# Kernel optimization log

Measured on AMD Instinct MI355X. Metric: run time of the kernel, lower is better.

Reference implementation:

```python
import jax, jax.numpy as jnp
import numpy as np

B, C, CI, H, W = 4, 256, 128, 64, 64  # batch, in_channels, inter_channels, spatial


def conv1x1(x, w, b):
    # x: [B,C,H,W], w: [O,C], b: [O] -> [B,O,H,W]
    return jnp.einsum('bchw,oc->bohw', x, w) + b[None, :, None, None]


def setup_inputs() -> dict:
    key = jax.random.key(0)
    ks = jax.random.split(key, 9)
    s = 0.02
    return {
        'x':  jax.random.normal(ks[0], (B, C, H, W), dtype=jnp.float32),
        'Wg': jax.random.normal(ks[1], (CI, C), dtype=jnp.float32) * s,
        'bg': jnp.zeros((CI,), dtype=jnp.float32),
        'Wt': jax.random.normal(ks[2], (CI, C), dtype=jnp.float32) * s,
        'bt': jnp.zeros((CI,), dtype=jnp.float32),
        'Wp': jax.random.normal(ks[3], (CI, C), dtype=jnp.float32) * s,
        'bp': jnp.zeros((CI,), dtype=jnp.float32),
        'Wo': jax.random.normal(ks[4], (C, CI), dtype=jnp.float32) * s,
        'bo': jnp.zeros((C,), dtype=jnp.float32),
    }


def reference(x, Wg, bg, Wt, bt, Wp, bp, Wo, bo):
    b, c, h, w = x.shape
    n = h * w
    g  = conv1x1(x, Wg, bg).reshape(b, -1, n)   # [B,CI,N]
    th = conv1x1(x, Wt, bt).reshape(b, -1, n)   # [B,CI,N]
    ph = conv1x1(x, Wp, bp).reshape(b, -1, n)   # [B,CI,N]
    f = jnp.einsum('bci,bcj->bij', th, ph)      # [B,N,N] unscaled scores
    a = jax.nn.softmax(f, axis=-1)
    y = jnp.einsum('bij,bcj->bci', a, g)        # [B,CI,N]
    y = y.reshape(b, -1, h, w)
    return conv1x1(y, Wo, bo) + x
```

## Files before the change

kernel.cpp:

```cpp
#include <hip/hip_runtime.h>
#include <math.h>

#define B_  4
#define C_  256
#define CI_ 128
#define N_  4096

typedef short s16x8  __attribute__((ext_vector_type(8)));
typedef float f32x4  __attribute__((ext_vector_type(4)));
typedef float f32x16 __attribute__((ext_vector_type(16)));

__device__ inline ushort f2bf(float f) {
    unsigned int u = __float_as_uint(f);
    u += 0x7FFF + ((u >> 16) & 1);
    return (ushort)(u >> 16);
}
__device__ inline float bf2f(ushort u) {
    return __uint_as_float(((unsigned int)u) << 16);
}

__device__ inline unsigned pkbf(float a, float b) {
    unsigned r;
    asm("v_cvt_pk_bf16_f32 %0, %1, %2" : "=v"(r) : "v"(a), "v"(b));
    return r;
}
__device__ inline void plswap(unsigned &x, unsigned &y) {
    asm volatile("v_permlane32_swap_b32 %0, %1" : "+v"(x), "+v"(y));
}

__device__ inline void gload_lds16(const void* g, void* l) {
    __builtin_amdgcn_global_load_lds(
        (const __attribute__((address_space(1))) unsigned int*)g,
        (__attribute__((address_space(3))) unsigned int*)l, 16, 0, 0);
}

__device__ inline void block_sync_lds() {
    asm volatile("s_waitcnt lgkmcnt(0)" ::: "memory");
    __builtin_amdgcn_s_barrier();
    asm volatile("" ::: "memory");
}

__global__ __launch_bounds__(256) void wcast_kernel(
    const float* __restrict__ Wg, const float* __restrict__ Wt,
    const float* __restrict__ Wp, const float* __restrict__ Wo,
    const float* __restrict__ bg, const float* __restrict__ bt,
    const float* __restrict__ bp,
    ushort* __restrict__ Wcat, ushort* __restrict__ Wobf,
    float* __restrict__ bcat)
{
    int i = blockIdx.x * 256 + threadIdx.x;
    if (i < 32768)       Wcat[i] = f2bf(Wg[i]);
    else if (i < 65536)  Wcat[i] = f2bf(Wt[i - 32768]);
    else if (i < 98304)  Wcat[i] = f2bf(Wp[i - 65536]);
    else if (i < 131072) Wobf[i - 98304] = f2bf(Wo[i - 98304]);
    if (i < 128)         bcat[i] = bg[i];
    else if (i < 256)    bcat[i] = bt[i - 128];
    else if (i < 384)    bcat[i] = bp[i - 256];
}

__global__ __launch_bounds__(256) void xt_kernel(
    const float* __restrict__ x, ushort* __restrict__ xT)
{
    __shared__ ushort Ls[64][72];
    const int b = blockIdx.z, c0 = blockIdx.y * 64, n0 = blockIdx.x * 64;
    const float* xb = x + ((size_t)b * C_ + c0) * N_ + n0;
    const int t = threadIdx.x;
    #pragma unroll
    for (int r = 0; r < 4; r++) {
        int idx = t + 256 * r;
        int c = idx >> 4, n4 = (idx & 15) * 4;
        float4 v = *(const float4*)&xb[(size_t)c * N_ + n4];
        ushort4 o;
        o.x = f2bf(v.x); o.y = f2bf(v.y); o.z = f2bf(v.z); o.w = f2bf(v.w);
        *(ushort4*)&Ls[c][n4] = o;
    }
    __syncthreads();
    ushort* xTb = xT + ((size_t)b * N_ + n0) * C_ + c0;
    #pragma unroll
    for (int r = 0; r < 2; r++) {
        int idx = t + 256 * r;
        int n = idx >> 3, c8 = (idx & 7) * 8;
        ushort tmp[8];
        #pragma unroll
        for (int u = 0; u < 8; u++) tmp[u] = Ls[c8 + u][n];
        *(uint4*)&xTb[(size_t)n * C_ + c8] = *(uint4*)tmp;
    }
}

__global__ __launch_bounds__(256) void proj_kernel(
    const ushort* __restrict__ Wcat, const float* __restrict__ bcat,
    const ushort* __restrict__ xT,
    ushort* __restrict__ g, ushort* __restrict__ tht, ushort* __restrict__ pht)
{
    __shared__ ushort Ws[64][72];
    __shared__ ushort Xs[64][72];
    const int b = blockIdx.z, mt = blockIdx.y, n0 = blockIdx.x * 64;
    const int t = threadIdx.x, wv = t >> 6, lane = t & 63;
    const int g4 = lane >> 4, ln = lane & 15;
    const ushort* Wsrc = Wcat + (size_t)mt * 64 * C_;
    const ushort* Xsrc = xT + ((size_t)b * N_ + n0) * C_;

    f32x4 acc[4];
    #pragma unroll
    for (int i = 0; i < 4; i++) acc[i] = (f32x4){0.f, 0.f, 0.f, 0.f};

    for (int k0 = 0; k0 < C_; k0 += 64) {
        block_sync_lds();
        #pragma unroll
        for (int r = 0; r < 2; r++) {
            int idx = t + 256 * r;
            int row = idx >> 3, k8 = (idx & 7) * 8;
            *(uint4*)&Ws[row][k8] = *(const uint4*)&Wsrc[(size_t)row * C_ + k0 + k8];
            *(uint4*)&Xs[row][k8] = *(const uint4*)&Xsrc[(size_t)row * C_ + k0 + k8];
        }
        block_sync_lds();
        if (mt < 2) {
            #pragma unroll
            for (int kk = 0; kk < 2; kk++) {
                s16x8 aW = *(const s16x8*)&Ws[16 * wv + ln][32 * kk + 8 * g4];
                #pragma unroll
                for (int nt = 0; nt < 4; nt++) {
                    s16x8 bX = *(const s16x8*)&Xs[16 * nt + ln][32 * kk + 8 * g4];
                    acc[nt] = __builtin_amdgcn_mfma_f32_16x16x32_bf16(aW, bX, acc[nt], 0, 0, 0);
                }
            }
        } else {
            #pragma unroll
            for (int kk = 0; kk < 2; kk++) {
                s16x8 aX = *(const s16x8*)&Xs[16 * wv + ln][32 * kk + 8 * g4];
                #pragma unroll
                for (int ct = 0; ct < 4; ct++) {
                    s16x8 bW = *(const s16x8*)&Ws[16 * ct + ln][32 * kk + 8 * g4];
                    acc[ct] = __builtin_amdgcn_mfma_f32_16x16x32_bf16(aX, bW, acc[ct], 0, 0, 0);
                }
            }
        }
    }

    if (mt < 2) {
        ushort* ob = g + (size_t)b * CI_ * N_;
        #pragma unroll
        for (int r = 0; r < 4; r++) {
            int mloc = 16 * wv + 4 * g4 + r;
            float bi = bcat[mt * 64 + mloc];
            #pragma unroll
            for (int nt = 0; nt < 4; nt++)
                ob[(size_t)(mt * 64 + mloc) * N_ + n0 + 16 * nt + ln] = f2bf(acc[nt][r] + bi);
        }
    } else {
        ushort* ob = ((mt < 4) ? tht : pht) + (size_t)b * N_ * CI_;
        int cib = ((mt - 2) & 1) * 64;
        #pragma unroll
        for (int r = 0; r < 4; r++) {
            int nloc = 16 * wv + 4 * g4 + r;
            #pragma unroll
            for (int ct = 0; ct < 4; ct++) {
                float bi = bcat[mt * 64 + 16 * ct + ln];
                ob[(size_t)(n0 + nloc) * CI_ + cib + 16 * ct + ln] = f2bf(acc[ct][r] + bi);
            }
        }
    }
}


__device__ inline float build_pa(const f32x16& S, s16x8& f0, s16x8& f1) {
    unsigned w[8];
    #pragma unroll
    for (int e = 0; e < 8; e++)
        w[e] = pkbf(__expf(S[2 * e]), __expf(S[2 * e + 1]));
    float ls = 0.f;
    #pragma unroll
    for (int e = 0; e < 8; e++)
        ls += __uint_as_float(w[e] << 16) + __uint_as_float(w[e] & 0xFFFF0000u);
    plswap(w[0], w[2]);
    plswap(w[1], w[3]);
    plswap(w[4], w[6]);
    plswap(w[5], w[7]);
    union { unsigned u[4]; s16x8 v; } A, B;
    A.u[0] = w[0]; A.u[1] = w[1]; A.u[2] = w[2]; A.u[3] = w[3];
    B.u[0] = w[4]; B.u[1] = w[5]; B.u[2] = w[6]; B.u[3] = w[7];
    f0 = A.v; f1 = B.v;
    return ls;
}

template <int NC>
__global__ __launch_bounds__(256, 3) void attn_mfma_kernel(
    const ushort* __restrict__ qn,
    const ushort* __restrict__ kn,
    const ushort* __restrict__ vm,
    ushort* __restrict__ Opart,
    float* __restrict__ lbuf)
{
    constexpr int JC = N_ / NC;
    __shared__ __align__(16) char smemB[32768];
    char* KsB = smemB;
    char* VtB = smemB + 16384;

    constexpr int NI = N_ / 128;
    constexpr int nb = NI * NC * B_;
    int flat = (blockIdx.z * NC + blockIdx.y) * NI + blockIdx.x;
    int nf   = (flat & 7) * (nb / 8) + (flat >> 3);
    const int i0    = (nf % NI) * 128;
    const int chunk = (nf / NI) % NC;
    const int b     = nf / (NI * NC);
    const int jbase = chunk * JC;

    const int t    = threadIdx.x;
    const int wv   = t >> 6;
    const int lane = t & 63;
    const int n32  = lane & 31;
    const int h    = lane >> 5;
    const int swz  = (n32 & 7) << 4;

    const ushort* qb = qn + ((size_t)b * N_ + i0) * CI_;
    const char* kB = (const char*)(kn + (size_t)b * N_ * CI_);
    const char* vB = (const char*)(vm + (size_t)b * CI_ * N_);

    s16x8 aQ[8];
    #pragma unroll
    for (int kk = 0; kk < 8; kk++)
        aQ[kk] = *(const s16x8*)(qb + (size_t)(32 * wv + n32) * CI_ + 16 * kk + 8 * h);

    f32x16 Oacc[4];
    #pragma unroll
    for (int dt = 0; dt < 4; dt++)
        #pragma unroll
        for (int e = 0; e < 16; e++) Oacc[dt][e] = 0.f;
    float lsum = 0.f;

    const int kr = lane >> 4;
    const int kc = (lane & 15) << 4;
    const int vr = lane >> 3;
    const int vc = (lane & 7) << 4;

    for (int jt = jbase; jt < jbase + JC; jt += 64) {
        block_sync_lds();

        #pragma unroll
        for (int r = 0; r < 4; r++) {
            int c   = (wv << 2) + r;
            int row = (c << 2) + kr;
            int src = ((jt + row) << 8) + (kc ^ ((row & 7) << 4));
            gload_lds16(kB + src, KsB + (c << 10));
        }
        #pragma unroll
        for (int r = 0; r < 4; r++) {
            int c   = (wv << 2) + r;
            int row = (c << 3) + vr;
            int src = row * (N_ * 2) + (jt << 1) + (vc ^ ((row & 7) << 4));
            gload_lds16(vB + src, VtB + (c << 10));
        }
        asm volatile("s_waitcnt vmcnt(0)" ::: "memory");
        __builtin_amdgcn_s_barrier();

        s16x8 pa[4];
        f32x16 S0;
        #pragma unroll
        for (int e = 0; e < 16; e++) S0[e] = 0.f;
        __builtin_amdgcn_s_setprio(1);
        #pragma unroll
        for (int kk = 0; kk < 8; kk++) {
            s16x8 aK0 = *(const s16x8*)(KsB + (n32 << 8) + (((kk << 5) + (h << 4)) ^ swz));
            S0 = __builtin_amdgcn_mfma_f32_32x32x16_bf16(aK0, aQ[kk], S0, 0, 0, 0);
        }
        __builtin_amdgcn_s_setprio(0);
        lsum += build_pa(S0, pa[0], pa[1]);

        f32x16 S1;
        #pragma unroll
        for (int e = 0; e < 16; e++) S1[e] = 0.f;
        __builtin_amdgcn_s_setprio(1);
        #pragma unroll
        for (int kk = 0; kk < 8; kk++) {
            s16x8 aK1 = *(const s16x8*)(KsB + 8192 + (n32 << 8) + (((kk << 5) + (h << 4)) ^ swz));
            S1 = __builtin_amdgcn_mfma_f32_32x32x16_bf16(aK1, aQ[kk], S1, 0, 0, 0);
        }
        __builtin_amdgcn_s_setprio(0);
        lsum += build_pa(S1, pa[2], pa[3]);

        __builtin_amdgcn_s_setprio(1);
        #pragma unroll
        for (int dt = 0; dt < 4; dt++) {
            #pragma unroll
            for (int kk = 0; kk < 4; kk++) {
                s16x8 bV = *(const s16x8*)(VtB + ((32 * dt + n32) << 7)
                                               + (((kk << 5) + (h << 4)) ^ swz));
                Oacc[dt] = __builtin_amdgcn_mfma_f32_32x32x16_bf16(pa[kk], bV, Oacc[dt], 0, 0, 0);
            }
        }
        __builtin_amdgcn_s_setprio(0);
    }

    ushort* Ob = Opart + (size_t)chunk * (B_ * N_ * CI_) + ((size_t)b * N_ + i0) * CI_;
    #pragma unroll
    for (int rg = 0; rg < 16; rg++) {
        int R = (rg & 3) + 8 * (rg >> 2) + 4 * h;
        int q = 32 * wv + R;
        #pragma unroll
        for (int dt = 0; dt < 4; dt++)
            Ob[(size_t)q * CI_ + 32 * dt + n32] = f2bf(Oacc[dt][rg]);
    }
    float ot  = __shfl_xor(lsum, 32);
    float tot = lsum + ot;
    if (h == 0)
        lbuf[((size_t)chunk * B_ + b) * N_ + i0 + 32 * wv + n32] = tot;
}

template <int NC>
__global__ __launch_bounds__(256) void outgemm_kernel(
    const ushort* __restrict__ Wobf, const float* __restrict__ bo,
    const ushort* __restrict__ Opart, const float* __restrict__ lbuf,
    const float* __restrict__ x, float* __restrict__ out)
{
    __shared__ ushort Ws[64][72];
    __shared__ ushort Ys[64][72];
    const int b = blockIdx.z, m0 = blockIdx.y * 64, n0 = blockIdx.x * 64;
    const int t = threadIdx.x, wv = t >> 6, lane = t & 63;
    const int g4 = lane >> 4, ln = lane & 15;
    const ushort* Wsrc = Wobf + (size_t)m0 * CI_;
    const size_t cs = (size_t)B_ * N_ * CI_;

    f32x4 acc[4];
    #pragma unroll
    for (int i = 0; i < 4; i++) acc[i] = (f32x4){0.f, 0.f, 0.f, 0.f};

    for (int k0 = 0; k0 < CI_; k0 += 64) {
        block_sync_lds();
        #pragma unroll
        for (int r = 0; r < 2; r++) {
            int idx = t + 256 * r;
            int row = idx >> 3, k8 = (idx & 7) * 8;
            *(uint4*)&Ws[row][k8] = *(const uint4*)&Wsrc[(size_t)row * CI_ + k0 + k8];
            size_t obase = ((size_t)b * N_ + n0 + row) * CI_ + k0 + k8;
            float lsum = 0.f;
            #pragma unroll
            for (int c = 0; c < NC; c++)
                lsum += lbuf[((size_t)c * B_ + b) * N_ + n0 + row];
            float inv = 1.0f / lsum;
            float osum[8];
            #pragma unroll
            for (int u = 0; u < 8; u++) osum[u] = 0.f;
            #pragma unroll
            for (int c = 0; c < NC; c++) {
                ushort oc[8];
                *(uint4*)oc = *(const uint4*)&Opart[(size_t)c * cs + obase];
                #pragma unroll
                for (int u = 0; u < 8; u++) osum[u] += bf2f(oc[u]);
            }
            ushort yo[8];
            #pragma unroll
            for (int u = 0; u < 8; u++) yo[u] = f2bf(osum[u] * inv);
            *(uint4*)&Ys[row][k8] = *(uint4*)yo;
        }
        block_sync_lds();
        #pragma unroll
        for (int kk = 0; kk < 2; kk++) {
            s16x8 aW = *(const s16x8*)&Ws[16 * wv + ln][32 * kk + 8 * g4];
            #pragma unroll
            for (int nt = 0; nt < 4; nt++) {
                s16x8 bY = *(const s16x8*)&Ys[16 * nt + ln][32 * kk + 8 * g4];
                acc[nt] = __builtin_amdgcn_mfma_f32_16x16x32_bf16(aW, bY, acc[nt], 0, 0, 0);
            }
        }
    }

    float* outb = out + (size_t)b * C_ * N_;
    const float* xb = x + (size_t)b * C_ * N_;
    #pragma unroll
    for (int r = 0; r < 4; r++) {
        int m = m0 + 16 * wv + 4 * g4 + r;
        float bi = bo[m];
        #pragma unroll
        for (int nt = 0; nt < 4; nt++) {
            size_t idx = (size_t)m * N_ + n0 + 16 * nt + ln;
            outb[idx] = acc[nt][r] + bi + xb[idx];
        }
    }
}

extern "C" void kernel_launch(void* const* d_in, const int* in_sizes, int n_in,
                              void* d_out, int out_size, void* d_ws, size_t ws_size,
                              hipStream_t stream) {
    const float* x  = (const float*)d_in[0];
    const float* Wg = (const float*)d_in[1];
    const float* bg = (const float*)d_in[2];
    const float* Wt = (const float*)d_in[3];
    const float* bt = (const float*)d_in[4];
    const float* Wp = (const float*)d_in[5];
    const float* bp = (const float*)d_in[6];
    const float* Wo = (const float*)d_in[7];
    const float* bo = (const float*)d_in[8];
    float* out = (float*)d_out;

    const bool big = ws_size >= 46925312ull;
    const int NC = big ? 8 : 4;

    char* w = (char*)d_ws;
    size_t opart_sz = (size_t)NC * B_ * N_ * CI_ * sizeof(ushort);
    ushort* xT    = (ushort*)w;
    ushort* Opart = (ushort*)w;
    ushort* g     = (ushort*)(w + opart_sz);
    ushort* tht   = (ushort*)(w + opart_sz + 4194304);
    ushort* pht   = (ushort*)(w + opart_sz + 8388608);
    ushort* Wcat  = (ushort*)(w + opart_sz + 12582912);
    ushort* Wobf  = (ushort*)(w + opart_sz + 12582912 + 196608);
    float*  bcat  = (float*) (w + opart_sz + 12582912 + 262144);
    float*  lbuf  = (float*) (w + opart_sz + 12582912 + 263680);

    dim3 blk(256);
    wcast_kernel<<<512, blk, 0, stream>>>(Wg, Wt, Wp, Wo, bg, bt, bp, Wcat, Wobf, bcat);
    xt_kernel<<<dim3(N_ / 64, C_ / 64, B_), blk, 0, stream>>>(x, xT);
    proj_kernel<<<dim3(N_ / 64, 6, B_), blk, 0, stream>>>(Wcat, bcat, xT, g, tht, pht);
    if (big) {
        attn_mfma_kernel<8><<<dim3(N_ / 128, 8, B_), blk, 0, stream>>>(tht, pht, g, Opart, lbuf);
        outgemm_kernel<8><<<dim3(N_ / 64, C_ / 64, B_), blk, 0, stream>>>(Wobf, bo, Opart, lbuf, x, out);
    } else {
        attn_mfma_kernel<4><<<dim3(N_ / 128, 4, B_), blk, 0, stream>>>(tht, pht, g, Opart, lbuf);
        outgemm_kernel<4><<<dim3(N_ / 64, C_ / 64, B_), blk, 0, stream>>>(Wobf, bo, Opart, lbuf, x, out);
    }
}
```

Measured before the change: 156.2 us.

## Double-buffer K/V tiles and process 64 queries per wave in attention

The attention kernel now gives each wave two 32-row query tiles, so every K/V fragment read from LDS feeds two MFMAs and the per-block query tile doubles to 256 rows. K/V staging is double-buffered in 64KB of LDS: the next tile's global-to-LDS loads are issued before computing on the current one, with a partial vmcnt wait. This targets LDS and global load traffic per MFMA and exposed load latency. In exchange it doubles the accumulator registers, halves the grid size, and lowers the occupancy target to 2 blocks per CU.

```diff
diff --git a/kernel.cpp b/kernel.cpp
--- a/kernel.cpp
+++ b/kernel.cpp
@@ -183,8 +183,25 @@
     return ls;
 }
 
+#define STAGE_KV(bufofs, jsrc) do {                                          \
+    _Pragma("unroll")                                                        \
+    for (int r_ = 0; r_ < 4; r_++) {                                         \
+        int c_   = (wv << 2) + r_;                                           \
+        int row_ = (c_ << 2) + kr;                                           \
+        int src_ = (((jsrc) + row_) << 8) + (kc ^ ((row_ & 7) << 4));        \
+        gload_lds16(kB + src_, smemB + (bufofs) + (c_ << 10));               \
+    }                                                                        \
+    _Pragma("unroll")                                                        \
+    for (int r_ = 0; r_ < 4; r_++) {                                         \
+        int c_   = (wv << 2) + r_;                                           \
+        int row_ = (c_ << 3) + vr;                                           \
+        int src_ = row_ * (N_ * 2) + ((jsrc) << 1) + (vc ^ ((row_ & 7) << 4));\
+        gload_lds16(vB + src_, smemB + (bufofs) + 16384 + (c_ << 10));       \
+    }                                                                        \
+} while (0)
+
 template <int NC>
-__global__ __launch_bounds__(256, 3) void attn_mfma_kernel(
+__global__ __launch_bounds__(256, 2) void attn_mfma_kernel(
     const ushort* __restrict__ qn,
     const ushort* __restrict__ kn,
     const ushort* __restrict__ vm,
@@ -192,15 +209,13 @@
     float* __restrict__ lbuf)
 {
     constexpr int JC = N_ / NC;
-    __shared__ __align__(16) char smemB[32768];
-    char* KsB = smemB;
-    char* VtB = smemB + 16384;
-
-    constexpr int NI = N_ / 128;
+    __shared__ __align__(16) char smemB[65536];
+
+    constexpr int NI = N_ / 256;
     constexpr int nb = NI * NC * B_;
     int flat = (blockIdx.z * NC + blockIdx.y) * NI + blockIdx.x;
     int nf   = (flat & 7) * (nb / 8) + (flat >> 3);
-    const int i0    = (nf % NI) * 128;
+    const int i0    = (nf % NI) * 256;
     const int chunk = (nf / NI) % NC;
     const int b     = nf / (NI * NC);
     const int jbase = chunk * JC;
@@ -212,98 +227,128 @@
     const int h    = lane >> 5;
     const int swz  = (n32 & 7) << 4;
 
-    const ushort* qb = qn + ((size_t)b * N_ + i0) * CI_;
     const char* kB = (const char*)(kn + (size_t)b * N_ * CI_);
     const char* vB = (const char*)(vm + (size_t)b * CI_ * N_);
 
-    s16x8 aQ[8];
-    #pragma unroll
-    for (int kk = 0; kk < 8; kk++)
-        aQ[kk] = *(const s16x8*)(qb + (size_t)(32 * wv + n32) * CI_ + 16 * kk + 8 * h);
-
-    f32x16 Oacc[4];
+    const ushort* qbw = qn + ((size_t)b * N_ + i0 + 64 * wv) * CI_;
+    s16x8 aQA[8], aQB[8];
+    #pragma unroll
+    for (int kk = 0; kk < 8; kk++) {
+        aQA[kk] = *(const s16x8*)(qbw + (size_t)n32 * CI_ + 16 * kk + 8 * h);
+        aQB[kk] = *(const s16x8*)(qbw + (size_t)(32 + n32) * CI_ + 16 * kk + 8 * h);
+    }
+
+    f32x16 OA[4], OB[4];
     #pragma unroll
     for (int dt = 0; dt < 4; dt++)
         #pragma unroll
-        for (int e = 0; e < 16; e++) Oacc[dt][e] = 0.f;
-    float lsum = 0.f;
+        for (int e = 0; e < 16; e++) { OA[dt][e] = 0.f; OB[dt][e] = 0.f; }
+    float lsA = 0.f, lsB = 0.f;
 
     const int kr = lane >> 4;
     const int kc = (lane & 15) << 4;
     const int vr = lane >> 3;
     const int vc = (lane & 7) << 4;
 
+    STAGE_KV(0, jbase);
+    int buf = 0;
     for (int jt = jbase; jt < jbase + JC; jt += 64) {
+        if (jt + 64 < jbase + JC) {
+            STAGE_KV(buf ^ 32768, jt + 64);
+            asm volatile("s_waitcnt vmcnt(8)" ::: "memory");
+        } else {
+            asm volatile("s_waitcnt vmcnt(0)" ::: "memory");
+        }
+        __builtin_amdgcn_s_barrier();
+        asm volatile("" ::: "memory");
+
+        const char* Kc = smemB + buf;
+        const char* Vc = smemB + buf + 16384;
+
+        {
+            f32x16 SA, SB;
+            #pragma unroll
+            for (int e = 0; e < 16; e++) { SA[e] = 0.f; SB[e] = 0.f; }
+            __builtin_amdgcn_s_setprio(1);
+            #pragma unroll
+            for (int kk = 0; kk < 8; kk++) {
+                s16x8 aK = *(const s16x8*)(Kc + (n32 << 8) + (((kk << 5) + (h << 4)) ^ swz));
+                SA = __builtin_amdgcn_mfma_f32_32x32x16_bf16(aK, aQA[kk], SA, 0, 0, 0);
+                SB = __builtin_amdgcn_mfma_f32_32x32x16_bf16(aK, aQB[kk], SB, 0, 0, 0);
+            }
+            __builtin_amdgcn_s_setprio(0);
+            s16x8 pA0, pA1, pB0, pB1;
+            lsA += build_pa(SA, pA0, pA1);
+            lsB += build_pa(SB, pB0, pB1);
+            __builtin_amdgcn_s_setprio(1);
+            #pragma unroll
+            for (int dt = 0; dt < 4; dt++) {
+                #pragma unroll
+                for (int kk = 0; kk < 2; kk++) {
+                    s16x8 bV = *(const s16x8*)(Vc + ((32 * dt + n32) << 7)
+                                                  + (((kk << 5) + (h << 4)) ^ swz));
+                    OA[dt] = __builtin_amdgcn_mfma_f32_32x32x16_bf16(
+                        kk == 0 ? pA0 : pA1, bV, OA[dt], 0, 0, 0);
+                    OB[dt] = __builtin_amdgcn_mfma_f32_32x32x16_bf16(
+                        kk == 0 ? pB0 : pB1, bV, OB[dt], 0, 0, 0);
+                }
+            }
+            __builtin_amdgcn_s_setprio(0);
+        }
+
+        {
+            f32x16 SA, SB;
+            #pragma unroll
+            for (int e = 0; e < 16; e++) { SA[e] = 0.f; SB[e] = 0.f; }
+            __builtin_amdgcn_s_setprio(1);
+            #pragma unroll
+            for (int kk = 0; kk < 8; kk++) {
+                s16x8 aK = *(const s16x8*)(Kc + 8192 + (n32 << 8) + (((kk << 5) + (h << 4)) ^ swz));
+                SA = __builtin_amdgcn_mfma_f32_32x32x16_bf16(aK, aQA[kk], SA, 0, 0, 0);
+                SB = __builtin_amdgcn_mfma_f32_32x32x16_bf16(aK, aQB[kk], SB, 0, 0, 0);
+            }
+            __builtin_amdgcn_s_setprio(0);
+            s16x8 pA2, pA3, pB2, pB3;
+            lsA += build_pa(SA, pA2, pA3);
+            lsB += build_pa(SB, pB2, pB3);
+            __builtin_amdgcn_s_setprio(1);
+            #pragma unroll
+            for (int dt = 0; dt < 4; dt++) {
+                #pragma unroll
+                for (int kk = 2; kk < 4; kk++) {
+                    s16x8 bV = *(const s16x8*)(Vc + ((32 * dt + n32) << 7)
+                                                  + (((kk << 5) + (h << 4)) ^ swz));
+                    OA[dt] = __builtin_amdgcn_mfma_f32_32x32x16_bf16(
+                        kk == 2 ? pA2 : pA3, bV, OA[dt], 0, 0, 0);
+                    OB[dt] = __builtin_amdgcn_mfma_f32_32x32x16_bf16(
+                        kk == 2 ? pB2 : pB3, bV, OB[dt], 0, 0, 0);
+                }
+            }
+            __builtin_amdgcn_s_setprio(0);
+        }
+
         block_sync_lds();
-
-        #pragma unroll
-        for (int r = 0; r < 4; r++) {
-            int c   = (wv << 2) + r;
-            int row = (c << 2) + kr;
-            int src = ((jt + row) << 8) + (kc ^ ((row & 7) << 4));
-            gload_lds16(kB + src, KsB + (c << 10));
-        }
-        #pragma unroll
-        for (int r = 0; r < 4; r++) {
-            int c   = (wv << 2) + r;
-            int row = (c << 3) + vr;
-            int src = row * (N_ * 2) + (jt << 1) + (vc ^ ((row & 7) << 4));
-            gload_lds16(vB + src, VtB + (c << 10));
-        }
-        asm volatile("s_waitcnt vmcnt(0)" ::: "memory");
-        __builtin_amdgcn_s_barrier();
-
-        s16x8 pa[4];
-        f32x16 S0;
-        #pragma unroll
-        for (int e = 0; e < 16; e++) S0[e] = 0.f;
-        __builtin_amdgcn_s_setprio(1);
-        #pragma unroll
-        for (int kk = 0; kk < 8; kk++) {
-            s16x8 aK0 = *(const s16x8*)(KsB + (n32 << 8) + (((kk << 5) + (h << 4)) ^ swz));
-            S0 = __builtin_amdgcn_mfma_f32_32x32x16_bf16(aK0, aQ[kk], S0, 0, 0, 0);
-        }
-        __builtin_amdgcn_s_setprio(0);
-        lsum += build_pa(S0, pa[0], pa[1]);
-
-        f32x16 S1;
-        #pragma unroll
-        for (int e = 0; e < 16; e++) S1[e] = 0.f;
-        __builtin_amdgcn_s_setprio(1);
-        #pragma unroll
-        for (int kk = 0; kk < 8; kk++) {
-            s16x8 aK1 = *(const s16x8*)(KsB + 8192 + (n32 << 8) + (((kk << 5) + (h << 4)) ^ swz));
-            S1 = __builtin_amdgcn_mfma_f32_32x32x16_bf16(aK1, aQ[kk], S1, 0, 0, 0);
-        }
-        __builtin_amdgcn_s_setprio(0);
-        lsum += build_pa(S1, pa[2], pa[3]);
-
-        __builtin_amdgcn_s_setprio(1);
-        #pragma unroll
-        for (int dt = 0; dt < 4; dt++) {
-            #pragma unroll
-            for (int kk = 0; kk < 4; kk++) {
-                s16x8 bV = *(const s16x8*)(VtB + ((32 * dt + n32) << 7)
-                                               + (((kk << 5) + (h << 4)) ^ swz));
-                Oacc[dt] = __builtin_amdgcn_mfma_f32_32x32x16_bf16(pa[kk], bV, Oacc[dt], 0, 0, 0);
-            }
-        }
-        __builtin_amdgcn_s_setprio(0);
-    }
-
-    ushort* Ob = Opart + (size_t)chunk * (B_ * N_ * CI_) + ((size_t)b * N_ + i0) * CI_;
+        buf ^= 32768;
+    }
+
+    ushort* Ob = Opart + (size_t)chunk * (B_ * N_ * CI_)
+                       + ((size_t)b * N_ + i0 + 64 * wv) * CI_;
     #pragma unroll
     for (int rg = 0; rg < 16; rg++) {
         int R = (rg & 3) + 8 * (rg >> 2) + 4 * h;
-        int q = 32 * wv + R;
-        #pragma unroll
-        for (int dt = 0; dt < 4; dt++)
-            Ob[(size_t)q * CI_ + 32 * dt + n32] = f2bf(Oacc[dt][rg]);
-    }
-    float ot  = __shfl_xor(lsum, 32);
-    float tot = lsum + ot;
-    if (h == 0)
-        lbuf[((size_t)chunk * B_ + b) * N_ + i0 + 32 * wv + n32] = tot;
+        #pragma unroll
+        for (int dt = 0; dt < 4; dt++) {
+            Ob[(size_t)R * CI_ + 32 * dt + n32]        = f2bf(OA[dt][rg]);
+            Ob[(size_t)(32 + R) * CI_ + 32 * dt + n32] = f2bf(OB[dt][rg]);
+        }
+    }
+    float totA = lsA + __shfl_xor(lsA, 32);
+    float totB = lsB + __shfl_xor(lsB, 32);
+    if (h == 0) {
+        float* lb = lbuf + ((size_t)chunk * B_ + b) * N_ + i0 + 64 * wv;
+        lb[n32]      = totA;
+        lb[32 + n32] = totB;
+    }
 }
 
 template <int NC>
@@ -412,10 +457,10 @@
     xt_kernel<<<dim3(N_ / 64, C_ / 64, B_), blk, 0, stream>>>(x, xT);
     proj_kernel<<<dim3(N_ / 64, 6, B_), blk, 0, stream>>>(Wcat, bcat, xT, g, tht, pht);
     if (big) {
-        attn_mfma_kernel<8><<<dim3(N_ / 128, 8, B_), blk, 0, stream>>>(tht, pht, g, Opart, lbuf);
+        attn_mfma_kernel<8><<<dim3(N_ / 256, 8, B_), blk, 0, stream>>>(tht, pht, g, Opart, lbuf);
         outgemm_kernel<8><<<dim3(N_ / 64, C_ / 64, B_), blk, 0, stream>>>(Wobf, bo, Opart, lbuf, x, out);
     } else {
-        attn_mfma_kernel<4><<<dim3(N_ / 128, 4, B_), blk, 0, stream>>>(tht, pht, g, Opart, lbuf);
+        attn_mfma_kernel<4><<<dim3(N_ / 256, 4, B_), blk, 0, stream>>>(tht, pht, g, Opart, lbuf);
         outgemm_kernel<4><<<dim3(N_ / 64, C_ / 64, B_), blk, 0, stream>>>(Wobf, bo, Opart, lbuf, x, out);
     }
 }
```

Result: slower. 189.1 us (+21.1%).
